# Kernel tuning notes

Measured on AMD Instinct MI355X. Metric: run time of the kernel, lower is better.

The kernel has to match this reference:

```python
import jax, jax.numpy as jnp
import numpy as np

B, L, D, H = 4, 2048, 1024, 16
HD = D // H
SCALE = 1.0 / (D / H) ** 0.5


def setup_inputs() -> dict:
    key = jax.random.key(0)
    ks = jax.random.split(key, 11)
    s = 1.0 / np.sqrt(D)
    return {
        "q": jax.random.normal(ks[0], (B, L, D), jnp.float32),
        "k": jax.random.normal(ks[1], (B, L, D), jnp.float32),
        "v": jax.random.normal(ks[2], (B, L, D), jnp.float32),
        "Wq": jax.random.normal(ks[3], (D, D), jnp.float32) * s,
        "bq": jnp.zeros((D,), jnp.float32),
        "Wk": jax.random.normal(ks[4], (D, D), jnp.float32) * s,
        "bk": jnp.zeros((D,), jnp.float32),
        "Wv": jax.random.normal(ks[5], (D, D), jnp.float32) * s,
        "bv": jnp.zeros((D,), jnp.float32),
        "Wo": jax.random.normal(ks[6], (D, D), jnp.float32) * s,
        "bo": jnp.zeros((D,), jnp.float32),
    }


def _split_heads(x):
    # [b, l, h*d] -> [b, h, l, d]
    b, l, _ = x.shape
    return x.reshape(b, l, H, HD).transpose(0, 2, 1, 3)


def reference(q, k, v, Wq, bq, Wk, bk, Wv, bv, Wo, bo):
    # Linear projections (torch Linear: x @ W.T + b)
    qh = _split_heads(q @ Wq.T + bq)            # [b, h, l, d]
    kh = _split_heads(k @ Wk.T + bk)            # [b, h, l, d]
    vh = _split_heads(v @ Wv.T + bv)            # [b, h, l, d]
    scores = jnp.einsum('bhqd,bhkd->bhqk', qh, kh) * SCALE
    attn = jax.nn.softmax(scores, axis=-1)       # dropout p=0 -> identity
    out = jnp.einsum('bhqk,bhkd->bhqd', attn, vh)
    out = out.transpose(0, 2, 1, 3).reshape(q.shape[0], q.shape[1], D)
    return out @ Wo.T + bo
```

## Files before the change

kernel.cpp:

```cpp
#include <hip/hip_runtime.h>


#define Bsz 4
#define Lq 2048
#define Dm 1024
#define NH 16
#define HD 64
#define QSCALE 0.18033688011112042f

typedef unsigned short u16;
typedef __attribute__((ext_vector_type(4))) short bf16x4;
typedef __attribute__((ext_vector_type(8))) short short8;
typedef __attribute__((ext_vector_type(4))) float f32x4;

#define MFMA32(a, b, c) __builtin_amdgcn_mfma_f32_16x16x32_bf16(a, b, c, 0, 0, 0)

typedef __attribute__((address_space(3))) unsigned su32;
typedef __attribute__((address_space(1))) unsigned gu32;
__device__ __forceinline__ void gl_lds16(const u16* g, u16* l) {
  __builtin_amdgcn_global_load_lds((gu32*)(g), (su32*)(l), 16, 0, 0);
}

__device__ __forceinline__ u16 f2b(float x) {
  unsigned u = __builtin_bit_cast(unsigned, x);
  return (u16)((u + 0x7fffu + ((u >> 16) & 1u)) >> 16);
}
__device__ __forceinline__ unsigned pk2(float a, float b) {
  return (unsigned)f2b(a) | ((unsigned)f2b(b) << 16);
}
__device__ __forceinline__ unsigned pk2p(float a, float b) {
  return __builtin_amdgcn_perm(__builtin_bit_cast(unsigned, b) + 0x8000u,
                               __builtin_bit_cast(unsigned, a) + 0x8000u, 0x07060302u);
}
__device__ __forceinline__ float fexp2(float x) {
#if __has_builtin(__builtin_amdgcn_exp2f)
  return __builtin_amdgcn_exp2f(x);
#else
  return exp2f(x);
#endif
}

__global__ void castk3(const float* __restrict__ q, const float* __restrict__ k,
                       const float* __restrict__ v, u16* __restrict__ dst) {
  const float* s = blockIdx.y == 0 ? q : (blockIdx.y == 1 ? k : v);
  u16* d = dst + (size_t)blockIdx.y * (Bsz * Lq * Dm);
  int i = (blockIdx.x * 256 + threadIdx.x) * 8;
  float4 a = *(const float4*)(s + i);
  float4 b = *(const float4*)(s + i + 4);
  short8 o;
  o[0] = (short)f2b(a.x); o[1] = (short)f2b(a.y);
  o[2] = (short)f2b(a.z); o[3] = (short)f2b(a.w);
  o[4] = (short)f2b(b.x); o[5] = (short)f2b(b.y);
  o[6] = (short)f2b(b.z); o[7] = (short)f2b(b.w);
  *(short8*)(d + i) = o;
}

__global__ void castw(const float* __restrict__ s0, const float* __restrict__ s1,
                      const float* __restrict__ s2, const float* __restrict__ s3,
                      u16* __restrict__ d0, u16* __restrict__ d1,
                      u16* __restrict__ d2, u16* __restrict__ d3) {
  const float* s; u16* d; float sc = 1.0f;
  switch (blockIdx.y) {
    case 0: s = s0; d = d0; sc = QSCALE; break;
    case 1: s = s1; d = d1; break;
    case 2: s = s2; d = d2; break;
    default: s = s3; d = d3; break;
  }
  int i = (blockIdx.x * 256 + threadIdx.x) * 8;
  float4 a = *(const float4*)(s + i);
  float4 b = *(const float4*)(s + i + 4);
  short8 o;
  o[0] = (short)f2b(a.x * sc); o[1] = (short)f2b(a.y * sc);
  o[2] = (short)f2b(a.z * sc); o[3] = (short)f2b(a.w * sc);
  o[4] = (short)f2b(b.x * sc); o[5] = (short)f2b(b.y * sc);
  o[6] = (short)f2b(b.z * sc); o[7] = (short)f2b(b.w * sc);
  *(short8*)(d + i) = o;
}

__global__ __launch_bounds__(256) void qkv_gemm(
    const u16* __restrict__ Ab,
    const u16* __restrict__ Wqb, const u16* __restrict__ Wkb, const u16* __restrict__ Wvb,
    const float* __restrict__ bq, const float* __restrict__ bk, const float* __restrict__ bv,
    u16* __restrict__ Qh, u16* __restrict__ Kh, u16* __restrict__ Vtg)
{
  __shared__ __align__(16) u16 As[128 * 32];
  __shared__ __align__(16) u16 Bs[128 * 32];
  const int z = blockIdx.z;
  const u16* A  = Ab + (size_t)z * (Bsz * Lq * Dm);
  const u16* Bt = z == 0 ? Wqb : (z == 1 ? Wkb : Wvb);
  const float* bias = z == 0 ? bq : (z == 1 ? bk : bv);
  const float bscale = z == 0 ? QSCALE : 1.0f;

  const int tid  = threadIdx.x;
  const int lane = tid & 63;
  const int wave = tid >> 6;
  const int quad = lane >> 4;
  const int r16  = lane & 15;
  const int wm   = (wave >> 1) * 64;
  const int wn   = (wave & 1) * 64;
  const int m0   = blockIdx.y * 128;
  const int n0   = blockIdx.x * 128;

  const u16* ga = A  + (size_t)(m0 + wave * 32 + (lane >> 2)) * Dm + (lane & 3) * 8;
  const u16* gb = Bt + (size_t)(n0 + wave * 32 + (lane >> 2)) * Dm + (lane & 3) * 8;
  u16* la = As + wave * 1024;
  u16* lb = Bs + wave * 1024;

  f32x4 acc[4][4] = {};

  for (int k0 = 0; k0 < Dm; k0 += 32) {
    gl_lds16(ga + k0, la);
    gl_lds16(ga + k0 + 16 * Dm, la + 512);
    gl_lds16(gb + k0, lb);
    gl_lds16(gb + k0 + 16 * Dm, lb + 512);
    __syncthreads();

    short8 af[4], bfr[4];
#pragma unroll
    for (int mt = 0; mt < 4; ++mt) af[mt]  = *(const short8*)&As[(wm + mt * 16 + r16) * 32 + quad * 8];
#pragma unroll
    for (int nt = 0; nt < 4; ++nt) bfr[nt] = *(const short8*)&Bs[(wn + nt * 16 + r16) * 32 + quad * 8];
#pragma unroll
    for (int mt = 0; mt < 4; ++mt)
#pragma unroll
      for (int nt = 0; nt < 4; ++nt)
        acc[mt][nt] = MFMA32(af[mt], bfr[nt], acc[mt][nt]);
    __syncthreads();
  }

#pragma unroll
  for (int mt = 0; mt < 4; ++mt) {
#pragma unroll
    for (int nt = 0; nt < 4; ++nt) {
      int n = n0 + wn + nt * 16 + r16;
      float bv_ = bias[n] * bscale;
      if (z == 2) {
        int m_base = m0 + wm + mt * 16 + quad * 4;
        int b = m_base >> 11, l0 = m_base & 2047;
        int lp = (l0 & ~31) | (((l0 >> 2) & 3) << 3) | (((l0 >> 4) & 1) << 2);
        int h = n >> 6, d = n & 63;
        u16* dst = Vtg + (((size_t)(b * NH + h)) * HD + d) * Lq + lp;
        uint2 pkd;
        pkd.x = pk2(acc[mt][nt][0] + bv_, acc[mt][nt][1] + bv_);
        pkd.y = pk2(acc[mt][nt][2] + bv_, acc[mt][nt][3] + bv_);
        *(uint2*)dst = pkd;
      } else {
        u16* dst = z == 0 ? Qh : Kh;
#pragma unroll
        for (int j = 0; j < 4; ++j) {
          int m = m0 + wm + mt * 16 + quad * 4 + j;
          int b = m >> 11, l = m & 2047;
          int h = n >> 6,  d = n & 63;
          dst[(((size_t)(b * NH + h)) * Lq + l) * HD + d] = f2b(acc[mt][nt][j] + bv_);
        }
      }
    }
  }
}

__global__ __launch_bounds__(256) void gemm_wo(
    const u16* __restrict__ A, const u16* __restrict__ Bt,
    const float* __restrict__ bias, float* __restrict__ C)
{
  __shared__ __align__(16) u16 As[128 * 32];
  __shared__ __align__(16) u16 Bs[64 * 32];
  const int tid  = threadIdx.x;
  const int lane = tid & 63;
  const int wave = tid >> 6;
  const int quad = lane >> 4;
  const int r16  = lane & 15;
  const int wm   = wave * 32;
  const int m0   = blockIdx.y * 128;
  const int n0   = blockIdx.x * 64;

  const u16* ga = A  + (size_t)(m0 + wave * 32 + (lane >> 2)) * Dm + (lane & 3) * 8;
  const u16* gb = Bt + (size_t)(n0 + wave * 16 + (lane >> 2)) * Dm + (lane & 3) * 8;
  u16* la = As + wave * 1024;
  u16* lb = Bs + wave * 512;

  f32x4 acc[2][4] = {};

  for (int k0 = 0; k0 < Dm; k0 += 32) {
    gl_lds16(ga + k0, la);
    gl_lds16(ga + k0 + 16 * Dm, la + 512);
    gl_lds16(gb + k0, lb);
    __syncthreads();

    short8 af[2], bfr[4];
#pragma unroll
    for (int mt = 0; mt < 2; ++mt) af[mt]  = *(const short8*)&As[(wm + mt * 16 + r16) * 32 + quad * 8];
#pragma unroll
    for (int nt = 0; nt < 4; ++nt) bfr[nt] = *(const short8*)&Bs[(nt * 16 + r16) * 32 + quad * 8];
#pragma unroll
    for (int mt = 0; mt < 2; ++mt)
#pragma unroll
      for (int nt = 0; nt < 4; ++nt)
        acc[mt][nt] = MFMA32(af[mt], bfr[nt], acc[mt][nt]);
    __syncthreads();
  }

#pragma unroll
  for (int mt = 0; mt < 2; ++mt) {
#pragma unroll
    for (int nt = 0; nt < 4; ++nt) {
      int n = n0 + nt * 16 + r16;
      float bv = bias[n];
#pragma unroll
      for (int j = 0; j < 4; ++j) {
        int m = m0 + wm + mt * 16 + quad * 4 + j;
        C[(size_t)m * Dm + n] = acc[mt][nt][j] + bv;
      }
    }
  }
}

__global__ __launch_bounds__(256) void attn4(
    const u16* __restrict__ Qh, const u16* __restrict__ Kh,
    const u16* __restrict__ Vtg, u16* __restrict__ Oa)
{
  const int bh = blockIdx.y;
  const int qt = blockIdx.x;
  const int tid = threadIdx.x, lane = tid & 63, wave = tid >> 6;
  const int quad = lane >> 4, r16 = lane & 15;

  __shared__ __align__(16) u16 Ks[64][64];
  __shared__ __align__(16) u16 Vt[64][64];

  const int qbase = qt * 128 + wave * 32;
  short8 aq[2][2];
#pragma unroll
  for (int qf = 0; qf < 2; ++qf) {
    const size_t qrow = ((size_t)bh * Lq + qbase + qf * 16 + r16) * HD;
    aq[qf][0] = *(const short8*)(Qh + qrow + quad * 8);
    aq[qf][1] = *(const short8*)(Qh + qrow + 32 + quad * 8);
  }

  f32x4 oacc[2][4] = {};
  float lsum[2] = {0.f, 0.f};

  const int srow = tid >> 2;
  const int sc0  = (tid & 3) * 2;
  const int ssw  = srow & 7;
  u16* kd0 = &Ks[srow][((sc0    ) ^ ssw) * 8];
  u16* kd1 = &Ks[srow][((sc0 + 1) ^ ssw) * 8];
  u16* vd0 = &Vt[srow][((sc0    ) ^ ssw) * 8];
  u16* vd1 = &Vt[srow][((sc0 + 1) ^ ssw) * 8];

  const u16* kg = Kh  + ((size_t)bh * Lq + srow) * HD + (tid & 3) * 16;
  const u16* vg = Vtg + ((size_t)bh * HD + srow) * Lq + (tid & 3) * 16;

  short8 pk0 = *(const short8*)(kg);
  short8 pk1 = *(const short8*)(kg + 8);
  short8 pv0 = *(const short8*)(vg);
  short8 pv1 = *(const short8*)(vg + 8);

  const int sx = r16 & 7;

  for (int t = 0; t < 32; ++t) {
    __syncthreads();
    *(short8*)kd0 = pk0;
    *(short8*)kd1 = pk1;
    *(short8*)vd0 = pv0;
    *(short8*)vd1 = pv1;
    __syncthreads();
    if (t < 31) {
      const u16* kgn = kg + (size_t)(t + 1) * 64 * HD;
      const u16* vgn = vg + (t + 1) * 64;
      pk0 = *(const short8*)(kgn);
      pk1 = *(const short8*)(kgn + 8);
      pv0 = *(const short8*)(vgn);
      pv1 = *(const short8*)(vgn + 8);
    }

#pragma unroll
    for (int ks = 0; ks < 2; ++ks) {
      f32x4 stq[2][2];
#pragma unroll
      for (int mtl = 0; mtl < 2; ++mtl) {
        const int mt = 2 * ks + mtl;
        short8 kf0 = *(const short8*)&Ks[mt * 16 + r16][((quad    ) ^ sx) * 8];
        short8 kf1 = *(const short8*)&Ks[mt * 16 + r16][((quad + 4) ^ sx) * 8];
#pragma unroll
        for (int qf = 0; qf < 2; ++qf) {
          f32x4 zz = {};
          zz = MFMA32(kf0, aq[qf][0], zz);
          zz = MFMA32(kf1, aq[qf][1], zz);
          stq[qf][mtl] = zz;
        }
      }
      short8 vf[4];
#pragma unroll
      for (int nt = 0; nt < 4; ++nt)
        vf[nt] = *(const short8*)&Vt[nt * 16 + r16][((ks * 4 + quad) ^ sx) * 8];
#pragma unroll
      for (int qf = 0; qf < 2; ++qf) {
        f32x4 sa = stq[qf][0], sb = stq[qf][1];
        float p0 = fexp2(sa[0]), p1 = fexp2(sa[1]), p2 = fexp2(sa[2]), p3 = fexp2(sa[3]);
        float p4 = fexp2(sb[0]), p5 = fexp2(sb[1]), p6 = fexp2(sb[2]), p7 = fexp2(sb[3]);
        lsum[qf] += ((p0 + p1) + (p2 + p3)) + ((p4 + p5) + (p6 + p7));
        uint4 pu;
        pu.x = pk2p(p0, p1);
        pu.y = pk2p(p2, p3);
        pu.z = pk2p(p4, p5);
        pu.w = pk2p(p6, p7);
        short8 pb = __builtin_bit_cast(short8, pu);
#pragma unroll
        for (int nt = 0; nt < 4; ++nt)
          oacc[qf][nt] = MFMA32(vf[nt], pb, oacc[qf][nt]);
      }
    }
  }

  const int b = bh >> 4, h = bh & 15;
  float linv[2];
#pragma unroll
  for (int qf = 0; qf < 2; ++qf) {
    float r = lsum[qf];
    r += __shfl_xor(r, 16);
    r += __shfl_xor(r, 32);
    linv[qf] = 1.0f / r;
  }
#pragma unroll
  for (int qf = 0; qf < 2; ++qf) {
    int q = qbase + qf * 16 + r16;
    size_t rowb = ((size_t)(b * Lq + q)) * Dm + h * HD;
#pragma unroll
    for (int nt = 0; nt < 4; ++nt) {
      f32x4 o = oacc[qf][nt];
      uint2 pkd;
      pkd.x = pk2(o[0] * linv[qf], o[1] * linv[qf]);
      pkd.y = pk2(o[2] * linv[qf], o[3] * linv[qf]);
      *(uint2*)&Oa[rowb + nt * 16 + quad * 4] = pkd;
    }
  }
}

extern "C" void kernel_launch(void* const* d_in, const int* in_sizes, int n_in,
                              void* d_out, int out_size, void* d_ws, size_t ws_size,
                              hipStream_t stream) {
  const float* q  = (const float*)d_in[0];
  const float* k  = (const float*)d_in[1];
  const float* v  = (const float*)d_in[2];
  const float* Wq = (const float*)d_in[3];
  const float* bq = (const float*)d_in[4];
  const float* Wk = (const float*)d_in[5];
  const float* bk = (const float*)d_in[6];
  const float* Wv = (const float*)d_in[7];
  const float* bv = (const float*)d_in[8];
  const float* Wo = (const float*)d_in[9];
  const float* bo = (const float*)d_in[10];

  const int NA = Bsz * Lq * Dm;
  u16* abuf = (u16*)d_ws;
  u16* Qh   = abuf + (size_t)3 * NA;
  u16* Kh   = Qh   + NA;
  u16* Vtg  = Kh   + NA;
  u16* wqb  = Vtg  + NA;
  u16* wkb  = wqb  + 1048576;
  u16* wvb  = wkb  + 1048576;
  u16* wob  = wvb  + 1048576;

  castw<<<dim3(512, 4), 256, 0, stream>>>(Wq, Wk, Wv, Wo, wqb, wkb, wvb, wob);
  castk3<<<dim3(NA / 2048, 3), 256, 0, stream>>>(q, k, v, abuf);

  qkv_gemm<<<dim3(8, 64, 3), 256, 0, stream>>>(abuf, wqb, wkb, wvb, bq, bk, bv, Qh, Kh, Vtg);

  attn4<<<dim3(Lq / 128, Bsz * NH), 256, 0, stream>>>(Qh, Kh, Vtg, abuf);

  gemm_wo<<<dim3(16, 64), 256, 0, stream>>>(abuf, wob, bo, (float*)d_out);
}
```

Measured before the change: 362.6 us.

## Double-buffer K/V tiles in LDS and compute row sums via MFMA

Splits the K and V shared-memory tiles into two buffers so the next tile is written into the idle buffer after compute. This cuts the per-iteration barriers from two to one. The softmax row-sum moves from scalar adds plus cross-lane shuffles to an extra MFMA against a vector of bf16 ones, so the sum is taken over the same bf16-rounded probabilities used in P·V. It also raises wave priority around the MFMA sections. The cost is twice the LDS per block, which may reduce occupancy, plus one extra MFMA per P tile.

Result: slower. 371.9 us (+2.6%).

```diff
diff --git a/kernel.cpp b/kernel.cpp
--- a/kernel.cpp
+++ b/kernel.cpp
@@ -223,8 +223,8 @@
   const int tid = threadIdx.x, lane = tid & 63, wave = tid >> 6;
   const int quad = lane >> 4, r16 = lane & 15;
 
-  __shared__ __align__(16) u16 Ks[64][64];
-  __shared__ __align__(16) u16 Vt[64][64];
+  __shared__ __align__(16) u16 Ks[2][64][64];
+  __shared__ __align__(16) u16 Vt[2][64][64];
 
   const int qbase = qt * 128 + wave * 32;
   short8 aq[2][2];
@@ -235,16 +235,18 @@
     aq[qf][1] = *(const short8*)(Qh + qrow + 32 + quad * 8);
   }
 
+  const short8 ones8 = {0x3F80, 0x3F80, 0x3F80, 0x3F80, 0x3F80, 0x3F80, 0x3F80, 0x3F80};
+
   f32x4 oacc[2][4] = {};
-  float lsum[2] = {0.f, 0.f};
+  f32x4 lacc[2] = {};
 
   const int srow = tid >> 2;
   const int sc0  = (tid & 3) * 2;
   const int ssw  = srow & 7;
-  u16* kd0 = &Ks[srow][((sc0    ) ^ ssw) * 8];
-  u16* kd1 = &Ks[srow][((sc0 + 1) ^ ssw) * 8];
-  u16* vd0 = &Vt[srow][((sc0    ) ^ ssw) * 8];
-  u16* vd1 = &Vt[srow][((sc0 + 1) ^ ssw) * 8];
+  const int wr0  = srow * 64 + ((sc0    ) ^ ssw) * 8;
+  const int wr1  = srow * 64 + ((sc0 + 1) ^ ssw) * 8;
+  u16* ksb = &Ks[0][0][0];
+  u16* vtb = &Vt[0][0][0];
 
   const u16* kg = Kh  + ((size_t)bh * Lq + srow) * HD + (tid & 3) * 16;
   const u16* vg = Vtg + ((size_t)bh * HD + srow) * Lq + (tid & 3) * 16;
@@ -254,15 +256,17 @@
   short8 pv0 = *(const short8*)(vg);
   short8 pv1 = *(const short8*)(vg + 8);
 
+  *(short8*)(ksb + wr0) = pk0;
+  *(short8*)(ksb + wr1) = pk1;
+  *(short8*)(vtb + wr0) = pv0;
+  *(short8*)(vtb + wr1) = pv1;
+  __syncthreads();
+
   const int sx = r16 & 7;
 
   for (int t = 0; t < 32; ++t) {
-    __syncthreads();
-    *(short8*)kd0 = pk0;
-    *(short8*)kd1 = pk1;
-    *(short8*)vd0 = pv0;
-    *(short8*)vd1 = pv1;
-    __syncthreads();
+    const int cur = (t & 1) * 4096;
+    const int nxt = 4096 - cur;
     if (t < 31) {
       const u16* kgn = kg + (size_t)(t + 1) * 64 * HD;
       const u16* vgn = vg + (t + 1) * 64;
@@ -275,11 +279,12 @@
 #pragma unroll
     for (int ks = 0; ks < 2; ++ks) {
       f32x4 stq[2][2];
+      __builtin_amdgcn_s_setprio(1);
 #pragma unroll
       for (int mtl = 0; mtl < 2; ++mtl) {
         const int mt = 2 * ks + mtl;
-        short8 kf0 = *(const short8*)&Ks[mt * 16 + r16][((quad    ) ^ sx) * 8];
-        short8 kf1 = *(const short8*)&Ks[mt * 16 + r16][((quad + 4) ^ sx) * 8];
+        short8 kf0 = *(const short8*)(ksb + cur + (mt * 16 + r16) * 64 + ((quad    ) ^ sx) * 8);
+        short8 kf1 = *(const short8*)(ksb + cur + (mt * 16 + r16) * 64 + ((quad + 4) ^ sx) * 8);
 #pragma unroll
         for (int qf = 0; qf < 2; ++qf) {
           f32x4 zz = {};
@@ -288,38 +293,44 @@
           stq[qf][mtl] = zz;
         }
       }
+      __builtin_amdgcn_s_setprio(0);
       short8 vf[4];
 #pragma unroll
       for (int nt = 0; nt < 4; ++nt)
-        vf[nt] = *(const short8*)&Vt[nt * 16 + r16][((ks * 4 + quad) ^ sx) * 8];
+        vf[nt] = *(const short8*)(vtb + cur + (nt * 16 + r16) * 64 + ((ks * 4 + quad) ^ sx) * 8);
 #pragma unroll
       for (int qf = 0; qf < 2; ++qf) {
         f32x4 sa = stq[qf][0], sb = stq[qf][1];
         float p0 = fexp2(sa[0]), p1 = fexp2(sa[1]), p2 = fexp2(sa[2]), p3 = fexp2(sa[3]);
         float p4 = fexp2(sb[0]), p5 = fexp2(sb[1]), p6 = fexp2(sb[2]), p7 = fexp2(sb[3]);
-        lsum[qf] += ((p0 + p1) + (p2 + p3)) + ((p4 + p5) + (p6 + p7));
         uint4 pu;
         pu.x = pk2p(p0, p1);
         pu.y = pk2p(p2, p3);
         pu.z = pk2p(p4, p5);
         pu.w = pk2p(p6, p7);
         short8 pb = __builtin_bit_cast(short8, pu);
+        __builtin_amdgcn_s_setprio(1);
+        lacc[qf] = MFMA32(ones8, pb, lacc[qf]);
 #pragma unroll
         for (int nt = 0; nt < 4; ++nt)
           oacc[qf][nt] = MFMA32(vf[nt], pb, oacc[qf][nt]);
+        __builtin_amdgcn_s_setprio(0);
       }
+    }
+
+    if (t < 31) {
+      *(short8*)(ksb + nxt + wr0) = pk0;
+      *(short8*)(ksb + nxt + wr1) = pk1;
+      *(short8*)(vtb + nxt + wr0) = pv0;
+      *(short8*)(vtb + nxt + wr1) = pv1;
+      __syncthreads();
     }
   }
 
   const int b = bh >> 4, h = bh & 15;
   float linv[2];
 #pragma unroll
-  for (int qf = 0; qf < 2; ++qf) {
-    float r = lsum[qf];
-    r += __shfl_xor(r, 16);
-    r += __shfl_xor(r, 32);
-    linv[qf] = 1.0f / r;
-  }
+  for (int qf = 0; qf < 2; ++qf) linv[qf] = 1.0f / lacc[qf][0];
 #pragma unroll
   for (int qf = 0; qf < 2; ++qf) {
     int q = qbase + qf * 16 + r16;
```
